# Kernel tuning notes

Measured on AMD Instinct MI355X. Metric: run time of the kernel, lower is better.

Reference implementation:

```python
import jax, jax.numpy as jnp
import numpy as np

NUM_SLOTS = 7
DIM = 4096
NUM_HEADS = 8
HEAD_DIM = DIM // NUM_HEADS
LN_EPS = 1e-5


def setup_inputs() -> dict:
    key = jax.random.key(0)
    ks = jax.random.split(key, 9)
    B, N = 8, 2048
    x = jax.random.normal(ks[0], (B, N, DIM), dtype=jnp.float32)
    slots = 1e-4 * jax.random.normal(ks[1], (NUM_SLOTS, DIM), dtype=jnp.float32)
    ln_g = jnp.ones((DIM,), jnp.float32)
    ln_b = jnp.zeros((DIM,), jnp.float32)
    # nn.MultiheadAttention packed in-projection: rows [Wq; Wk; Wv], each (DIM, DIM)
    s = 1.0 / np.sqrt(DIM)
    in_proj_w = jax.random.uniform(ks[2], (3 * DIM, DIM), jnp.float32, -s, s)
    in_proj_b = jnp.zeros((3 * DIM,), jnp.float32)
    out_proj_w = jax.random.uniform(ks[3], (DIM, DIM), jnp.float32, -s, s)
    out_proj_b = jnp.zeros((DIM,), jnp.float32)
    alpha = 0.1 * jax.random.normal(ks[4], (1,), jnp.float32)  # nonzero so gate path is active
    return {"x": x, "slots": slots, "ln_g": ln_g, "ln_b": ln_b,
            "in_proj_w": in_proj_w, "in_proj_b": in_proj_b,
            "out_proj_w": out_proj_w, "out_proj_b": out_proj_b, "alpha": alpha}


def _cmrm(x, slots, ln_g, ln_b, in_proj_w, in_proj_b, out_proj_w, out_proj_b, alpha):
    x32 = x.astype(jnp.float32)
    # pre LayerNorm
    mu = jnp.mean(x32, axis=-1, keepdims=True)
    var = jnp.mean(jnp.square(x32 - mu), axis=-1, keepdims=True)
    xn = (x32 - mu) * jax.lax.rsqrt(var + LN_EPS) * ln_g + ln_b  # (B,N,D)
    slots_c = jnp.clip(slots, -10.0, 10.0)  # (Q,D), Q=7
    Wq, Wk, Wv = jnp.split(in_proj_w, 3, axis=0)
    bq, bk, bv = jnp.split(in_proj_b, 3, axis=0)
    q = slots_c @ Wq.T + bq                      # (Q,D), identical for all batches
    k = xn @ Wk.T + bk                           # (B,N,D)
    v = xn @ Wv.T + bv                           # (B,N,D)
    B, N, _ = x.shape
    qh = q.reshape(NUM_SLOTS, NUM_HEADS, HEAD_DIM)          # (Q,H,hd)
    kh = k.reshape(B, N, NUM_HEADS, HEAD_DIM)
    vh = v.reshape(B, N, NUM_HEADS, HEAD_DIM)
    scale = 1.0 / np.sqrt(HEAD_DIM)
    scores = jnp.einsum('qhd,bnhd->bhqn', qh * scale, kh)   # (B,H,Q,N)
    attn = jax.nn.softmax(scores, axis=-1)
    ctx = jnp.einsum('bhqn,bnhd->bqhd', attn, vh).reshape(B, NUM_SLOTS, DIM)
    slots_out = ctx @ out_proj_w.T + out_proj_b             # (B,Q,D)
    slots_res = slots_c[None] + slots_out                   # residual, ungated slots
    gate = jnp.tanh(alpha)                                  # (1,)
    g = jnp.mean(gate * slots_res, axis=1, keepdims=True)   # (B,1,D)
    x_refined = (x32 + g).astype(x.dtype)
    attn_weights = jnp.mean(attn, axis=1)                   # torch avg over heads -> (B,Q,N)
    return x_refined, attn_weights


def reference(x, slots, ln_g, ln_b, in_proj_w, in_proj_b, out_proj_w, out_proj_b, alpha):
    return _cmrm(x, slots, ln_g, ln_b, in_proj_w, in_proj_b, out_proj_w, out_proj_b, alpha)
```

## Files before the change

### kernel.cpp

```cpp
#include <hip/hip_runtime.h>

typedef __attribute__((ext_vector_type(4))) float f32x4;
typedef __attribute__((ext_vector_type(8))) short short8x;

#define DIM   4096
#define NB    8
#define NN    2048
#define NROWS (NB*NN)
#define NHD   8
#define NQ    7
#define NHQ   56
#define SCALE 0.04419417382415922f

#define OFF_MU     0L
#define OFF_RSTD   16384L
#define OFF_Q7     32768L
#define OFF_SC7    61440L
#define OFF_U56    90112L
#define OFF_A      319488L
#define OFF_D0     319552L
#define OFF_SM     319616L
#define OFF_S1     323712L
#define OFF_CTXM   323776L
#define OFF_GFIN   356544L
#define OFF_YM     389312L
#define OFF_UGBF   651456L
#define OFF_STATP  782528L
#define OFF_SCT    913600L
#define OFF_BIG    1962176L
#define OFF_ATTN   (OFF_BIG)
#define OFF_AM     (OFF_BIG + 917504L)
#define OFF_PART   (OFF_BIG + 1048576L)

__device__ __forceinline__ unsigned short f2bf(float f) {
  union { float f; unsigned int u; } v; v.f = f;
  return (unsigned short)((v.u + 0x7FFFu + ((v.u >> 16) & 1u)) >> 16);
}
__device__ __forceinline__ unsigned short f2bfr(float f) {
  union { float f; unsigned int u; } v; v.f = f;
  return (unsigned short)((v.u + 0x8000u) >> 16);
}

__device__ __forceinline__ float blockSum256(float v, float* red) {
  #pragma unroll
  for (int m = 1; m < 64; m <<= 1) v += __shfl_xor(v, m);
  __syncthreads();
  if ((threadIdx.x & 63) == 0) red[threadIdx.x >> 6] = v;
  __syncthreads();
  return red[0] + red[1] + red[2] + red[3];
}
__device__ __forceinline__ float blockMax256(float v, float* red) {
  #pragma unroll
  for (int m = 1; m < 64; m <<= 1) v = fmaxf(v, __shfl_xor(v, m));
  __syncthreads();
  if ((threadIdx.x & 63) == 0) red[threadIdx.x >> 6] = v;
  __syncthreads();
  return fmaxf(fmaxf(red[0], red[1]), fmaxf(red[2], red[3]));
}

__global__ __launch_bounds__(256) void k_smean(const float* __restrict__ slots,
    float* __restrict__ sm, float* __restrict__ sc7) {
  int e = blockIdx.x * 256 + threadIdx.x;
  float s = 0;
  #pragma unroll
  for (int q = 0; q < 7; q++) {
    float v = fminf(fmaxf(slots[(long)q*DIM + e], -10.0f), 10.0f);
    sc7[(long)q*DIM + e] = v;
    s += v;
  }
  sm[e] = s * (1.0f / 7.0f);
}

__global__ __launch_bounds__(256) void k_qproj(const float* __restrict__ ipw,
    const float* __restrict__ ipb, const float* __restrict__ sc7, float* __restrict__ q7) {
  const int w = threadIdx.x >> 6, l = threadIdx.x & 63;
  const int d = blockIdx.x * 4 + w;
  const float4* wr4 = (const float4*)(ipw + (long)d * DIM);
  float acc[7] = {0,0,0,0,0,0,0};
  for (int e4 = l; e4 < 1024; e4 += 64) {
    float4 wv = wr4[e4];
    #pragma unroll
    for (int s = 0; s < 7; s++) {
      float4 sv = ((const float4*)(sc7 + (long)s*DIM))[e4];
      acc[s] += wv.x*sv.x + wv.y*sv.y + wv.z*sv.z + wv.w*sv.w;
    }
  }
  #pragma unroll
  for (int s = 0; s < 7; s++) {
    #pragma unroll
    for (int m = 1; m < 64; m <<= 1) acc[s] += __shfl_xor(acc[s], m);
  }
  if (l == 0) {
    float bq = ipb[d];
    #pragma unroll
    for (int s = 0; s < 7; s++) q7[(long)s*DIM + d] = acc[s] + bq;
  }
}

__global__ __launch_bounds__(256) void k_uproj(const float* __restrict__ ipw,
    const float* __restrict__ q7, float* __restrict__ upart) {
  const int h = blockIdx.y, c = blockIdx.z;
  const int e = blockIdx.x * 256 + threadIdx.x;
  __shared__ float qs[7][128];
  for (int i = threadIdx.x; i < 7*128; i += 256) {
    int s = i >> 7, hd = i & 127;
    qs[s][hd] = q7[(long)s*DIM + h*512 + c*128 + hd];
  }
  __syncthreads();
  float acc[7] = {0,0,0,0,0,0,0};
  const float* wp = ipw + ((long)(DIM + h*512 + c*128))*DIM + e;
  for (int hd = 0; hd < 128; hd++) {
    float wv = wp[(long)hd * DIM];
    #pragma unroll
    for (int s = 0; s < 7; s++) acc[s] += qs[s][hd] * wv;
  }
  #pragma unroll
  for (int s = 0; s < 7; s++) upart[(long)((c*8 + h)*7 + s)*DIM + e] = acc[s];
}

__global__ __launch_bounds__(256) void k_ured(const float* __restrict__ upart,
    const float* __restrict__ lng, float* __restrict__ u56, unsigned short* __restrict__ ugbf) {
  const int h = blockIdx.y;
  const int e = blockIdx.x * 256 + threadIdx.x;
  if (h == 8) {
    #pragma unroll
    for (int r = 0; r < 8; r++) ugbf[(long)(56 + r)*DIM + e] = 0;
    return;
  }
  float ge = lng[e];
  #pragma unroll
  for (int s = 0; s < 7; s++) {
    float u = 0;
    #pragma unroll
    for (int c = 0; c < 4; c++) u += upart[(long)((c*8 + h)*7 + s)*DIM + e];
    u *= SCALE;
    u56[(long)(h*7 + s)*DIM + e] = u;
    ugbf[(long)(h*7 + s)*DIM + e] = f2bf(u * ge);
  }
}

__global__ __launch_bounds__(256) void k_ad(const float* __restrict__ u56,
    const float* __restrict__ q7, const float* __restrict__ lng, const float* __restrict__ lnb,
    const float* __restrict__ ipb, float* __restrict__ Aarr, float* __restrict__ D0arr) {
  __shared__ float red[4];
  const int hq = blockIdx.x, h = hq / 7, q = hq % 7;
  float pa = 0, pd = 0, pc = 0;
  for (int e = threadIdx.x; e < DIM; e += 256) {
    float uv = u56[(long)hq*DIM + e];
    pa += uv * lng[e]; pd += uv * lnb[e];
  }
  for (int hd = threadIdx.x; hd < 512; hd += 256)
    pc += q7[(long)q*DIM + h*512 + hd] * ipb[DIM + h*512 + hd];
  pa = blockSum256(pa, red);
  pd = blockSum256(pd, red);
  pc = blockSum256(pc, red);
  if (threadIdx.x == 0) { Aarr[hq] = pa; D0arr[hq] = pd + SCALE * pc; }
}

__global__ __launch_bounds__(256) void k_scores2(const float* __restrict__ x,
    const unsigned short* __restrict__ ugbf, float* __restrict__ raw, float2* __restrict__ statp) {
  const int tid = threadIdx.x;
  const int w = tid >> 6, l = tid & 63;
  const int lr = l & 15, lk8 = (l >> 4) * 8;
  const int rowblk = blockIdx.x >> 2, ks = blockIdx.x & 3;
  const int row0w = rowblk * 64 + w * 16;
  const long arow = (long)(row0w + lr) * DIM;
  const int kbase = ks * 1024;
  f32x4 acc0 = {0,0,0,0}, acc1 = {0,0,0,0}, acc2 = {0,0,0,0}, acc3 = {0,0,0,0};
  float sx = 0.f, sxx = 0.f;
  const long b0 = (long)(0*16 + lr)*DIM, b1 = (long)(1*16 + lr)*DIM,
             b2 = (long)(2*16 + lr)*DIM, b3 = (long)(3*16 + lr)*DIM;
  #pragma unroll 2
  for (int kc = kbase; kc < kbase + 1024; kc += 32) {
    const float4 v0 = *(const float4*)(x + arow + kc + lk8);
    const float4 v1 = *(const float4*)(x + arow + kc + lk8 + 4);
    sx  += (v0.x + v0.y) + (v0.z + v0.w) + (v1.x + v1.y) + (v1.z + v1.w);
    sxx += v0.x*v0.x + v0.y*v0.y + v0.z*v0.z + v0.w*v0.w
         + v1.x*v1.x + v1.y*v1.y + v1.z*v1.z + v1.w*v1.w;
    short8x a;
    a[0] = (short)f2bfr(v0.x); a[1] = (short)f2bfr(v0.y);
    a[2] = (short)f2bfr(v0.z); a[3] = (short)f2bfr(v0.w);
    a[4] = (short)f2bfr(v1.x); a[5] = (short)f2bfr(v1.y);
    a[6] = (short)f2bfr(v1.z); a[7] = (short)f2bfr(v1.w);
    short8x bb0 = *(const short8x*)(ugbf + b0 + kc + lk8);
    acc0 = __builtin_amdgcn_mfma_f32_16x16x32_bf16(a, bb0, acc0, 0, 0, 0);
    short8x bb1 = *(const short8x*)(ugbf + b1 + kc + lk8);
    acc1 = __builtin_amdgcn_mfma_f32_16x16x32_bf16(a, bb1, acc1, 0, 0, 0);
    short8x bb2 = *(const short8x*)(ugbf + b2 + kc + lk8);
    acc2 = __builtin_amdgcn_mfma_f32_16x16x32_bf16(a, bb2, acc2, 0, 0, 0);
    short8x bb3 = *(const short8x*)(ugbf + b3 + kc + lk8);
    acc3 = __builtin_amdgcn_mfma_f32_16x16x32_bf16(a, bb3, acc3, 0, 0, 0);
  }
  sx += __shfl_xor(sx, 16);  sx += __shfl_xor(sx, 32);
  sxx += __shfl_xor(sxx, 16); sxx += __shfl_xor(sxx, 32);
  if (l < 16) {
    float2 p; p.x = sx; p.y = sxx;
    statp[(long)ks*NROWS + row0w + l] = p;
  }
  const long base = ((long)ks*NROWS + row0w) * 64;
  #pragma unroll
  for (int i = 0; i < 4; i++) {
    long ro = base + (long)((l >> 4)*4 + i) * 64 + lr;
    raw[ro +  0] = acc0[i];
    raw[ro + 16] = acc1[i];
    raw[ro + 32] = acc2[i];
    raw[ro + 48] = acc3[i];
  }
}

__global__ __launch_bounds__(256) void k_sepi(const float* __restrict__ raw,
    const float2* __restrict__ statp, const float* __restrict__ Aarr,
    const float* __restrict__ D0arr, float* __restrict__ mu_o, float* __restrict__ rstd_o,
    float* __restrict__ sct) {
  const int w = threadIdx.x >> 6, l = threadIdx.x & 63;
  const int row = blockIdx.x * 4 + w;
  float s = 0;
  #pragma unroll
  for (int ks = 0; ks < 4; ks++) s += raw[((long)ks*NROWS + row)*64 + l];
  float sx = 0, sxx = 0;
  #pragma unroll
  for (int ks = 0; ks < 4; ks++) {
    float2 p = statp[(long)ks*NROWS + row];
    sx += p.x; sxx += p.y;
  }
  float mu = sx * (1.0f/DIM), var = sxx * (1.0f/DIM) - mu*mu;
  float rs = rsqrtf(var + 1e-5f);
  if (l == 0) { mu_o[row] = mu; rstd_o[row] = rs; }
  if (l < NHQ) sct[(long)l*NROWS + row] = rs*(s - mu*Aarr[l]) + D0arr[l];
}

__global__ __launch_bounds__(256) void k_softmax(const float* __restrict__ sct,
    float* __restrict__ attn) {
  __shared__ float red[4];
  const int b = blockIdx.x / NHQ, hq = blockIdx.x % NHQ;
  const int tid = threadIdx.x;
  const float* sp = sct + (long)hq*NROWS + (long)b*NN;
  float s[8]; float mx = -3.4e38f;
  #pragma unroll
  for (int j = 0; j < 8; j++) { s[j] = sp[tid + j*256]; mx = fmaxf(mx, s[j]); }
  mx = blockMax256(mx, red);
  float sum = 0;
  #pragma unroll
  for (int j = 0; j < 8; j++) { s[j] = __expf(s[j] - mx); sum += s[j]; }
  sum = blockSum256(sum, red);
  float inv = 1.0f / sum;
  const int h = hq / NQ, q = hq % NQ;
  float* ap = attn + ((long)(b*NHD + h)*NQ + q)*NN;
  #pragma unroll
  for (int j = 0; j < 8; j++) ap[tid + j*256] = s[j] * inv;
}

__global__ __launch_bounds__(256) void k_means(const float* __restrict__ attn,
    float* __restrict__ am, float* __restrict__ out_attn) {
  const int b = blockIdx.x >> 3, nc = blockIdx.x & 7;
  const int n = nc*256 + threadIdx.x;
  float aq[7] = {0,0,0,0,0,0,0};
  #pragma unroll
  for (int h = 0; h < 8; h++) {
    float ah = 0;
    #pragma unroll
    for (int q = 0; q < 7; q++) {
      float v = attn[((long)(b*NHD + h)*NQ + q)*NN + n];
      aq[q] += v; ah += v;
    }
    am[((long)(b*NHD + h))*NN + n] = ah * (1.0f/7.0f);
  }
  #pragma unroll
  for (int q = 0; q < 7; q++) out_attn[((long)(b*NQ + q))*NN + n] = aq[q] * 0.125f;
}

__global__ __launch_bounds__(256) void k_s1(const float* __restrict__ am,
    const float* __restrict__ mu, const float* __restrict__ rstd, float* __restrict__ s1) {
  __shared__ float red[4];
  const int bh = blockIdx.x, b = bh >> 3;
  float p = 0;
  for (int n = threadIdx.x; n < NN; n += 256) {
    int row = b*NN + n;
    p += am[(long)bh*NN + n] * mu[row] * rstd[row];
  }
  p = blockSum256(p, red);
  if (threadIdx.x == 0) s1[bh] = p;
}

__global__ __launch_bounds__(256) void k_ypart(const float* __restrict__ x,
    const float* __restrict__ am, const float* __restrict__ rstd, float* __restrict__ part) {
  const int bid = blockIdx.x;
  const int b = bid >> 6, ec = (bid >> 4) & 3, nc = bid & 15;
  __shared__ float amr[8][128];
  const int tid = threadIdx.x;
  for (int i = tid; i < 1024; i += 256) {
    int h = i >> 7, nn = i & 127;
    int row = b*NN + nc*128 + nn;
    amr[h][nn] = am[((long)(b*NHD + h))*NN + nc*128 + nn] * rstd[row];
  }
  __syncthreads();
  const int e = ec*1024 + tid*4;
  float ax[8], ay[8], az[8], aw[8];
  #pragma unroll
  for (int h = 0; h < 8; h++) { ax[h]=0; ay[h]=0; az[h]=0; aw[h]=0; }
  const float* xp = x + ((long)(b*NN + nc*128))*DIM + e;
  #pragma unroll 2
  for (int nn = 0; nn < 128; nn++) {
    const float4 xv = *(const float4*)(xp + (long)nn*DIM);
    #pragma unroll
    for (int h = 0; h < 8; h++) {
      float a = amr[h][nn];
      ax[h] += a*xv.x; ay[h] += a*xv.y; az[h] += a*xv.z; aw[h] += a*xv.w;
    }
  }
  #pragma unroll
  for (int h = 0; h < 8; h++) {
    float4 o; o.x = ax[h]; o.y = ay[h]; o.z = az[h]; o.w = aw[h];
    *(float4*)&part[((long)(nc*64 + b*8 + h))*DIM + e] = o;
  }
}

__global__ __launch_bounds__(256) void k_yred(const float* __restrict__ part,
    const float* __restrict__ s1, const float* __restrict__ lng, const float* __restrict__ lnb,
    float* __restrict__ ym) {
  const long i4 = (long)blockIdx.x*256 + threadIdx.x;
  const float4* p4 = (const float4*)part;
  float4 s = p4[i4];
  #pragma unroll
  for (int nc = 1; nc < 16; nc++) {
    float4 v = p4[(long)nc*65536 + i4];
    s.x += v.x; s.y += v.y; s.z += v.z; s.w += v.w;
  }
  const int bh = (int)(i4 >> 10), e4 = (int)(i4 & 1023);
  float sv = s1[bh];
  float4 g = ((const float4*)lng)[e4], bb = ((const float4*)lnb)[e4];
  float4 o;
  o.x = g.x*(s.x - sv) + bb.x; o.y = g.y*(s.y - sv) + bb.y;
  o.z = g.z*(s.z - sv) + bb.z; o.w = g.w*(s.w - sv) + bb.w;
  ((float4*)ym)[i4] = o;
}

__global__ __launch_bounds__(256) void k_ctxm(const float* __restrict__ ipw,
    const float* __restrict__ ipb, const float* __restrict__ ym, float* __restrict__ ctxm) {
  const int w = threadIdx.x >> 6, l = threadIdx.x & 63;
  const int d = blockIdx.x*4 + w;
  const int h = d >> 9;
  const float4* wr4 = (const float4*)(ipw + ((long)(2*DIM + d))*DIM);
  float acc[8] = {0,0,0,0,0,0,0,0};
  for (int e4 = l; e4 < 1024; e4 += 64) {
    float4 wv = wr4[e4];
    #pragma unroll
    for (int b = 0; b < 8; b++) {
      float4 y = ((const float4*)(ym + (long)(b*8 + h)*DIM))[e4];
      acc[b] += wv.x*y.x + wv.y*y.y + wv.z*y.z + wv.w*y.w;
    }
  }
  #pragma unroll
  for (int b = 0; b < 8; b++) {
    #pragma unroll
    for (int m = 1; m < 64; m <<= 1) acc[b] += __shfl_xor(acc[b], m);
  }
  if (l == 0) {
    float bias = ipb[2*DIM + d];
    #pragma unroll
    for (int b = 0; b < 8; b++) ctxm[(long)b*DIM + d] = acc[b] + bias;
  }
}

__global__ __launch_bounds__(256) void k_gvec(const float* __restrict__ opw,
    const float* __restrict__ opb, const float* __restrict__ ctxm, const float* __restrict__ sm,
    const float* __restrict__ alpha, float* __restrict__ gfin) {
  const int w = threadIdx.x >> 6, l = threadIdx.x & 63;
  const int d = blockIdx.x*4 + w;
  const float4* wr4 = (const float4*)(opw + (long)d*DIM);
  float acc[8] = {0,0,0,0,0,0,0,0};
  for (int e4 = l; e4 < 1024; e4 += 64) {
    float4 wv = wr4[e4];
    #pragma unroll
    for (int b = 0; b < 8; b++) {
      float4 c = ((const float4*)(ctxm + (long)b*DIM))[e4];
      acc[b] += wv.x*c.x + wv.y*c.y + wv.z*c.z + wv.w*c.w;
    }
  }
  #pragma unroll
  for (int b = 0; b < 8; b++) {
    #pragma unroll
    for (int m = 1; m < 64; m <<= 1) acc[b] += __shfl_xor(acc[b], m);
  }
  if (l == 0) {
    float t = tanhf(alpha[0]);
    float base = sm[d] + opb[d];
    #pragma unroll
    for (int b = 0; b < 8; b++) gfin[(long)b*DIM + d] = t * (base + acc[b]);
  }
}

__global__ __launch_bounds__(256) void k_refine(const float* __restrict__ x,
    const float* __restrict__ gfin, float* __restrict__ out) {
  const float4* x4 = (const float4*)x;
  const float4* g4 = (const float4*)gfin;
  float4* o4 = (float4*)out;
  const long total = (long)NROWS * 1024;
  for (long i4 = (long)blockIdx.x*256 + threadIdx.x; i4 < total; i4 += (long)gridDim.x*256) {
    long b = i4 >> 21;
    long e4 = i4 & 1023;
    float4 xv = x4[i4], gv = g4[b*1024 + e4];
    float4 o; o.x = xv.x + gv.x; o.y = xv.y + gv.y; o.z = xv.z + gv.z; o.w = xv.w + gv.w;
    o4[i4] = o;
  }
}

extern "C" void kernel_launch(void* const* d_in, const int* in_sizes, int n_in,
                              void* d_out, int out_size, void* d_ws, size_t ws_size,
                              hipStream_t stream) {
  const float* x     = (const float*)d_in[0];
  const float* slots = (const float*)d_in[1];
  const float* lng   = (const float*)d_in[2];
  const float* lnb   = (const float*)d_in[3];
  const float* ipw   = (const float*)d_in[4];
  const float* ipb   = (const float*)d_in[5];
  const float* opw   = (const float*)d_in[6];
  const float* opb   = (const float*)d_in[7];
  const float* alpha = (const float*)d_in[8];
  float* out = (float*)d_out;
  float* ws  = (float*)d_ws;

  float* mu     = ws + OFF_MU;
  float* rstd   = ws + OFF_RSTD;
  float* q7     = ws + OFF_Q7;
  float* sc7    = ws + OFF_SC7;
  float* u56    = ws + OFF_U56;
  float* Aarr   = ws + OFF_A;
  float* D0arr  = ws + OFF_D0;
  float* sm     = ws + OFF_SM;
  float* s1     = ws + OFF_S1;
  float* ctxm   = ws + OFF_CTXM;
  float* gfin   = ws + OFF_GFIN;
  float* ym     = ws + OFF_YM;
  unsigned short* ugbf = (unsigned short*)(ws + OFF_UGBF);
  float2* statp = (float2*)(ws + OFF_STATP);
  float* sct    = ws + OFF_SCT;
  float* upart  = ws + OFF_BIG;
  float* raw    = ws + OFF_BIG;
  float* attn   = ws + OFF_ATTN;
  float* am     = ws + OFF_AM;
  float* part   = ws + OFF_PART;
  float* out_attn = out + (long)NROWS * DIM;

  hipLaunchKernelGGL(k_smean,   dim3(16),        dim3(256), 0, stream, slots, sm, sc7);
  hipLaunchKernelGGL(k_qproj,   dim3(1024),      dim3(256), 0, stream, ipw, ipb, sc7, q7);
  hipLaunchKernelGGL(k_uproj,   dim3(16, 8, 4),  dim3(256), 0, stream, ipw, q7, upart);
  hipLaunchKernelGGL(k_ured,    dim3(16, 9),     dim3(256), 0, stream, upart, lng, u56, ugbf);
  hipLaunchKernelGGL(k_ad,      dim3(56),        dim3(256), 0, stream, u56, q7, lng, lnb, ipb, Aarr, D0arr);
  hipLaunchKernelGGL(k_scores2, dim3(1024),      dim3(256), 0, stream, x, ugbf, raw, statp);
  hipLaunchKernelGGL(k_sepi,    dim3(4096),      dim3(256), 0, stream, raw, statp, Aarr, D0arr, mu, rstd, sct);
  hipLaunchKernelGGL(k_softmax, dim3(448),       dim3(256), 0, stream, sct, attn);
  hipLaunchKernelGGL(k_means,   dim3(64),        dim3(256), 0, stream, attn, am, out_attn);
  hipLaunchKernelGGL(k_s1,      dim3(64),        dim3(256), 0, stream, am, mu, rstd, s1);
  hipLaunchKernelGGL(k_ypart,   dim3(512),       dim3(256), 0, stream, x, am, rstd, part);
  hipLaunchKernelGGL(k_yred,    dim3(256),       dim3(256), 0, stream, part, s1, lng, lnb, ym);
  hipLaunchKernelGGL(k_ctxm,    dim3(1024),      dim3(256), 0, stream, ipw, ipb, ym, ctxm);
  hipLaunchKernelGGL(k_gvec,    dim3(1024),      dim3(256), 0, stream, opw, opb, ctxm, sm, alpha, gfin);
  hipLaunchKernelGGL(k_refine,  dim3(8192),      dim3(256), 0, stream, x, gfin, out);
}
```

Baseline: 406.4 us.

## Fuse small kernels and recompute softmax probabilities instead of materializing attn

Folds the slot clamp and mean into the q-projection and gvec kernels, merges the A/D0 reductions into k_ured via atomics, and replaces the full softmax write plus separate means and s1 kernels with a stats-only softmax followed by a fused kernel that recomputes probabilities and accumulates head means and s1. It also doubles the number of ypart blocks by halving the row chunk. The aim is to cut launch count and the round trip of the large attn intermediate. In exchange it adds float atomics, which make the summation order nondeterministic, and redoes the exp work in the second pass.

Result: slower. 425.3 us (+4.6%).

```diff
diff --git a/kernel.cpp b/kernel.cpp
--- a/kernel.cpp
+++ b/kernel.cpp
@@ -15,22 +15,19 @@
 #define OFF_MU     0L
 #define OFF_RSTD   16384L
 #define OFF_Q7     32768L
-#define OFF_SC7    61440L
-#define OFF_U56    90112L
-#define OFF_A      319488L
-#define OFF_D0     319552L
-#define OFF_SM     319616L
-#define OFF_S1     323712L
-#define OFF_CTXM   323776L
-#define OFF_GFIN   356544L
-#define OFF_YM     389312L
-#define OFF_UGBF   651456L
-#define OFF_STATP  782528L
-#define OFF_SCT    913600L
-#define OFF_BIG    1962176L
-#define OFF_ATTN   (OFF_BIG)
-#define OFF_AM     (OFF_BIG + 917504L)
-#define OFF_PART   (OFF_BIG + 1048576L)
+#define OFF_A      61440L
+#define OFF_D0     61504L
+#define OFF_S1     61568L
+#define OFF_SMST   61632L
+#define OFF_CTXM   62528L
+#define OFF_GFIN   95296L
+#define OFF_YM     128064L
+#define OFF_UGBF   390208L
+#define OFF_STATP  521280L
+#define OFF_SCT    652352L
+#define OFF_BIG    1700928L
+#define OFF_AM     (OFF_BIG)
+#define OFF_PART   (OFF_BIG + 131072L)
 
 __device__ __forceinline__ unsigned short f2bf(float f) {
   union { float f; unsigned int u; } v; v.f = f;
@@ -41,9 +38,13 @@
   return (unsigned short)((v.u + 0x8000u) >> 16);
 }
 
+__device__ __forceinline__ float waveSum(float v) {
+  #pragma unroll
+  for (int m = 1; m < 64; m <<= 1) v += __shfl_xor(v, m);
+  return v;
+}
 __device__ __forceinline__ float blockSum256(float v, float* red) {
-  #pragma unroll
-  for (int m = 1; m < 64; m <<= 1) v += __shfl_xor(v, m);
+  v = waveSum(v);
   __syncthreads();
   if ((threadIdx.x & 63) == 0) red[threadIdx.x >> 6] = v;
   __syncthreads();
@@ -58,21 +59,8 @@
   return fmaxf(fmaxf(red[0], red[1]), fmaxf(red[2], red[3]));
 }
 
-__global__ __launch_bounds__(256) void k_smean(const float* __restrict__ slots,
-    float* __restrict__ sm, float* __restrict__ sc7) {
-  int e = blockIdx.x * 256 + threadIdx.x;
-  float s = 0;
-  #pragma unroll
-  for (int q = 0; q < 7; q++) {
-    float v = fminf(fmaxf(slots[(long)q*DIM + e], -10.0f), 10.0f);
-    sc7[(long)q*DIM + e] = v;
-    s += v;
-  }
-  sm[e] = s * (1.0f / 7.0f);
-}
-
 __global__ __launch_bounds__(256) void k_qproj(const float* __restrict__ ipw,
-    const float* __restrict__ ipb, const float* __restrict__ sc7, float* __restrict__ q7) {
+    const float* __restrict__ ipb, const float* __restrict__ slots, float* __restrict__ q7) {
   const int w = threadIdx.x >> 6, l = threadIdx.x & 63;
   const int d = blockIdx.x * 4 + w;
   const float4* wr4 = (const float4*)(ipw + (long)d * DIM);
@@ -81,20 +69,29 @@
     float4 wv = wr4[e4];
     #pragma unroll
     for (int s = 0; s < 7; s++) {
-      float4 sv = ((const float4*)(sc7 + (long)s*DIM))[e4];
+      float4 sv = ((const float4*)(slots + (long)s*DIM))[e4];
+      sv.x = fminf(fmaxf(sv.x, -10.f), 10.f); sv.y = fminf(fmaxf(sv.y, -10.f), 10.f);
+      sv.z = fminf(fmaxf(sv.z, -10.f), 10.f); sv.w = fminf(fmaxf(sv.w, -10.f), 10.f);
       acc[s] += wv.x*sv.x + wv.y*sv.y + wv.z*sv.z + wv.w*sv.w;
     }
   }
   #pragma unroll
-  for (int s = 0; s < 7; s++) {
-    #pragma unroll
-    for (int m = 1; m < 64; m <<= 1) acc[s] += __shfl_xor(acc[s], m);
-  }
+  for (int s = 0; s < 7; s++) acc[s] = waveSum(acc[s]);
   if (l == 0) {
     float bq = ipb[d];
     #pragma unroll
     for (int s = 0; s < 7; s++) q7[(long)s*DIM + d] = acc[s] + bq;
   }
+}
+
+__global__ __launch_bounds__(64) void k_adinit(const float* __restrict__ q7,
+    const float* __restrict__ ipb, float* __restrict__ Aarr, float* __restrict__ D0arr) {
+  const int hq = blockIdx.x, h = hq / 7, q = hq % 7;
+  float acc = 0;
+  for (int i = threadIdx.x; i < 512; i += 64)
+    acc += q7[(long)q*DIM + h*512 + i] * ipb[DIM + h*512 + i];
+  acc = waveSum(acc);
+  if (threadIdx.x == 0) { Aarr[hq] = 0.f; D0arr[hq] = SCALE * acc; }
 }
 
 __global__ __launch_bounds__(256) void k_uproj(const float* __restrict__ ipw,
@@ -119,7 +116,8 @@
 }
 
 __global__ __launch_bounds__(256) void k_ured(const float* __restrict__ upart,
-    const float* __restrict__ lng, float* __restrict__ u56, unsigned short* __restrict__ ugbf) {
+    const float* __restrict__ lng, const float* __restrict__ lnb,
+    unsigned short* __restrict__ ugbf, float* __restrict__ Aarr, float* __restrict__ D0arr) {
   const int h = blockIdx.y;
   const int e = blockIdx.x * 256 + threadIdx.x;
   if (h == 8) {
@@ -127,34 +125,21 @@
     for (int r = 0; r < 8; r++) ugbf[(long)(56 + r)*DIM + e] = 0;
     return;
   }
-  float ge = lng[e];
+  float ge = lng[e], be = lnb[e];
   #pragma unroll
   for (int s = 0; s < 7; s++) {
     float u = 0;
     #pragma unroll
     for (int c = 0; c < 4; c++) u += upart[(long)((c*8 + h)*7 + s)*DIM + e];
     u *= SCALE;
-    u56[(long)(h*7 + s)*DIM + e] = u;
     ugbf[(long)(h*7 + s)*DIM + e] = f2bf(u * ge);
-  }
-}
-
-__global__ __launch_bounds__(256) void k_ad(const float* __restrict__ u56,
-    const float* __restrict__ q7, const float* __restrict__ lng, const float* __restrict__ lnb,
-    const float* __restrict__ ipb, float* __restrict__ Aarr, float* __restrict__ D0arr) {
-  __shared__ float red[4];
-  const int hq = blockIdx.x, h = hq / 7, q = hq % 7;
-  float pa = 0, pd = 0, pc = 0;
-  for (int e = threadIdx.x; e < DIM; e += 256) {
-    float uv = u56[(long)hq*DIM + e];
-    pa += uv * lng[e]; pd += uv * lnb[e];
-  }
-  for (int hd = threadIdx.x; hd < 512; hd += 256)
-    pc += q7[(long)q*DIM + h*512 + hd] * ipb[DIM + h*512 + hd];
-  pa = blockSum256(pa, red);
-  pd = blockSum256(pd, red);
-  pc = blockSum256(pc, red);
-  if (threadIdx.x == 0) { Aarr[hq] = pa; D0arr[hq] = pd + SCALE * pc; }
+    float pa = waveSum(u * ge);
+    float pd = waveSum(u * be);
+    if ((threadIdx.x & 63) == 0) {
+      atomicAdd(&Aarr[h*7 + s], pa);
+      atomicAdd(&D0arr[h*7 + s], pd);
+    }
+  }
 }
 
 __global__ __launch_bounds__(256) void k_scores2(const float* __restrict__ x,
@@ -229,9 +214,10 @@
   if (l < NHQ) sct[(long)l*NROWS + row] = rs*(s - mu*Aarr[l]) + D0arr[l];
 }
 
-__global__ __launch_bounds__(256) void k_softmax(const float* __restrict__ sct,
-    float* __restrict__ attn) {
+__global__ __launch_bounds__(256) void k_smax(const float* __restrict__ sct,
+    float2* __restrict__ stats, float* __restrict__ s1) {
   __shared__ float red[4];
+  if (blockIdx.x == 0 && threadIdx.x < 64) s1[threadIdx.x] = 0.f;
   const int b = blockIdx.x / NHQ, hq = blockIdx.x % NHQ;
   const int tid = threadIdx.x;
   const float* sp = sct + (long)hq*NROWS + (long)b*NN;
@@ -241,66 +227,59 @@
   mx = blockMax256(mx, red);
   float sum = 0;
   #pragma unroll
-  for (int j = 0; j < 8; j++) { s[j] = __expf(s[j] - mx); sum += s[j]; }
+  for (int j = 0; j < 8; j++) sum += __expf(s[j] - mx);
   sum = blockSum256(sum, red);
-  float inv = 1.0f / sum;
-  const int h = hq / NQ, q = hq % NQ;
-  float* ap = attn + ((long)(b*NHD + h)*NQ + q)*NN;
-  #pragma unroll
-  for (int j = 0; j < 8; j++) ap[tid + j*256] = s[j] * inv;
-}
-
-__global__ __launch_bounds__(256) void k_means(const float* __restrict__ attn,
-    float* __restrict__ am, float* __restrict__ out_attn) {
+  if (tid == 0) { float2 o; o.x = mx; o.y = 1.0f/sum; stats[b*NHQ + hq] = o; }
+}
+
+__global__ __launch_bounds__(256) void k_attnmeans(const float* __restrict__ sct,
+    const float2* __restrict__ stats, const float* __restrict__ mu, const float* __restrict__ rstd,
+    float* __restrict__ am, float* __restrict__ s1, float* __restrict__ out_attn) {
   const int b = blockIdx.x >> 3, nc = blockIdx.x & 7;
-  const int n = nc*256 + threadIdx.x;
+  const int tid = threadIdx.x;
+  const int n = nc*256 + tid, row = b*NN + n;
+  __shared__ float2 st[56];
+  if (tid < 56) st[tid] = stats[b*NHQ + tid];
+  __syncthreads();
+  const float mur = mu[row] * rstd[row];
   float aq[7] = {0,0,0,0,0,0,0};
   #pragma unroll
   for (int h = 0; h < 8; h++) {
     float ah = 0;
     #pragma unroll
     for (int q = 0; q < 7; q++) {
-      float v = attn[((long)(b*NHD + h)*NQ + q)*NN + n];
-      aq[q] += v; ah += v;
-    }
-    am[((long)(b*NHD + h))*NN + n] = ah * (1.0f/7.0f);
+      float2 s2 = st[h*7 + q];
+      float p = __expf(sct[(long)(h*7 + q)*NROWS + row] - s2.x) * s2.y;
+      aq[q] += p; ah += p;
+    }
+    float amv = ah * (1.0f/7.0f);
+    am[((long)(b*8 + h))*NN + n] = amv;
+    float sv = waveSum(amv * mur);
+    if ((tid & 63) == 0) atomicAdd(&s1[b*8 + h], sv);
   }
   #pragma unroll
   for (int q = 0; q < 7; q++) out_attn[((long)(b*NQ + q))*NN + n] = aq[q] * 0.125f;
-}
-
-__global__ __launch_bounds__(256) void k_s1(const float* __restrict__ am,
-    const float* __restrict__ mu, const float* __restrict__ rstd, float* __restrict__ s1) {
-  __shared__ float red[4];
-  const int bh = blockIdx.x, b = bh >> 3;
-  float p = 0;
-  for (int n = threadIdx.x; n < NN; n += 256) {
-    int row = b*NN + n;
-    p += am[(long)bh*NN + n] * mu[row] * rstd[row];
-  }
-  p = blockSum256(p, red);
-  if (threadIdx.x == 0) s1[bh] = p;
 }
 
 __global__ __launch_bounds__(256) void k_ypart(const float* __restrict__ x,
     const float* __restrict__ am, const float* __restrict__ rstd, float* __restrict__ part) {
   const int bid = blockIdx.x;
-  const int b = bid >> 6, ec = (bid >> 4) & 3, nc = bid & 15;
-  __shared__ float amr[8][128];
+  const int b = bid >> 7, ec = (bid >> 5) & 3, nc = bid & 31;
+  __shared__ float amr[8][64];
   const int tid = threadIdx.x;
-  for (int i = tid; i < 1024; i += 256) {
-    int h = i >> 7, nn = i & 127;
-    int row = b*NN + nc*128 + nn;
-    amr[h][nn] = am[((long)(b*NHD + h))*NN + nc*128 + nn] * rstd[row];
+  for (int i = tid; i < 512; i += 256) {
+    int h = i >> 6, nn = i & 63;
+    int row = b*NN + nc*64 + nn;
+    amr[h][nn] = am[((long)(b*8 + h))*NN + nc*64 + nn] * rstd[row];
   }
   __syncthreads();
   const int e = ec*1024 + tid*4;
   float ax[8], ay[8], az[8], aw[8];
   #pragma unroll
   for (int h = 0; h < 8; h++) { ax[h]=0; ay[h]=0; az[h]=0; aw[h]=0; }
-  const float* xp = x + ((long)(b*NN + nc*128))*DIM + e;
+  const float* xp = x + ((long)(b*NN + nc*64))*DIM + e;
   #pragma unroll 2
-  for (int nn = 0; nn < 128; nn++) {
+  for (int nn = 0; nn < 64; nn++) {
     const float4 xv = *(const float4*)(xp + (long)nn*DIM);
     #pragma unroll
     for (int h = 0; h < 8; h++) {
@@ -322,7 +301,7 @@
   const float4* p4 = (const float4*)part;
   float4 s = p4[i4];
   #pragma unroll
-  for (int nc = 1; nc < 16; nc++) {
+  for (int nc = 1; nc < 32; nc++) {
     float4 v = p4[(long)nc*65536 + i4];
     s.x += v.x; s.y += v.y; s.z += v.z; s.w += v.w;
   }
@@ -351,10 +330,7 @@
     }
   }
   #pragma unroll
-  for (int b = 0; b < 8; b++) {
-    #pragma unroll
-    for (int m = 1; m < 64; m <<= 1) acc[b] += __shfl_xor(acc[b], m);
-  }
+  for (int b = 0; b < 8; b++) acc[b] = waveSum(acc[b]);
   if (l == 0) {
     float bias = ipb[2*DIM + d];
     #pragma unroll
@@ -363,7 +339,7 @@
 }
 
 __global__ __launch_bounds__(256) void k_gvec(const float* __restrict__ opw,
-    const float* __restrict__ opb, const float* __restrict__ ctxm, const float* __restrict__ sm,
+    const float* __restrict__ opb, const float* __restrict__ ctxm, const float* __restrict__ slots,
     const float* __restrict__ alpha, float* __restrict__ gfin) {
   const int w = threadIdx.x >> 6, l = threadIdx.x & 63;
   const int d = blockIdx.x*4 + w;
@@ -378,13 +354,15 @@
     }
   }
   #pragma unroll
-  for (int b = 0; b < 8; b++) {
-    #pragma unroll
-    for (int m = 1; m < 64; m <<= 1) acc[b] += __shfl_xor(acc[b], m);
-  }
+  for (int b = 0; b < 8; b++) acc[b] = waveSum(acc[b]);
   if (l == 0) {
+    float smv = 0;
+    #pragma unroll
+    for (int q = 0; q < 7; q++)
+      smv += fminf(fmaxf(slots[(long)q*DIM + d], -10.f), 10.f);
+    smv *= (1.0f/7.0f);
     float t = tanhf(alpha[0]);
-    float base = sm[d] + opb[d];
+    float base = smv + opb[d];
     #pragma unroll
     for (int b = 0; b < 8; b++) gfin[(long)b*DIM + d] = t * (base + acc[b]);
   }
@@ -423,12 +401,10 @@
   float* mu     = ws + OFF_MU;
   float* rstd   = ws + OFF_RSTD;
   float* q7     = ws + OFF_Q7;
-  float* sc7    = ws + OFF_SC7;
-  float* u56    = ws + OFF_U56;
   float* Aarr   = ws + OFF_A;
   float* D0arr  = ws + OFF_D0;
-  float* sm     = ws + OFF_SM;
   float* s1     = ws + OFF_S1;
+  float2* stats = (float2*)(ws + OFF_SMST);
   float* ctxm   = ws + OFF_CTXM;
   float* gfin   = ws + OFF_GFIN;
   float* ym     = ws + OFF_YM;
@@ -437,24 +413,21 @@
   float* sct    = ws + OFF_SCT;
   float* upart  = ws + OFF_BIG;
   float* raw    = ws + OFF_BIG;
-  float* attn   = ws + OFF_ATTN;
   float* am     = ws + OFF_AM;
   float* part   = ws + OFF_PART;
   float* out_attn = out + (long)NROWS * DIM;
 
-  hipLaunchKernelGGL(k_smean,   dim3(16),        dim3(256), 0, stream, slots, sm, sc7);
-  hipLaunchKernelGGL(k_qproj,   dim3(1024),      dim3(256), 0, stream, ipw, ipb, sc7, q7);
-  hipLaunchKernelGGL(k_uproj,   dim3(16, 8, 4),  dim3(256), 0, stream, ipw, q7, upart);
-  hipLaunchKernelGGL(k_ured,    dim3(16, 9),     dim3(256), 0, stream, upart, lng, u56, ugbf);
-  hipLaunchKernelGGL(k_ad,      dim3(56),        dim3(256), 0, stream, u56, q7, lng, lnb, ipb, Aarr, D0arr);
-  hipLaunchKernelGGL(k_scores2, dim3(1024),      dim3(256), 0, stream, x, ugbf, raw, statp);
-  hipLaunchKernelGGL(k_sepi,    dim3(4096),      dim3(256), 0, stream, raw, statp, Aarr, D0arr, mu, rstd, sct);
-  hipLaunchKernelGGL(k_softmax, dim3(448),       dim3(256), 0, stream, sct, attn);
-  hipLaunchKernelGGL(k_means,   dim3(64),        dim3(256), 0, stream, attn, am, out_attn);
-  hipLaunchKernelGGL(k_s1,      dim3(64),        dim3(256), 0, stream, am, mu, rstd, s1);
-  hipLaunchKernelGGL(k_ypart,   dim3(512),       dim3(256), 0, stream, x, am, rstd, part);
-  hipLaunchKernelGGL(k_yred,    dim3(256),       dim3(256), 0, stream, part, s1, lng, lnb, ym);
-  hipLaunchKernelGGL(k_ctxm,    dim3(1024),      dim3(256), 0, stream, ipw, ipb, ym, ctxm);
-  hipLaunchKernelGGL(k_gvec,    dim3(1024),      dim3(256), 0, stream, opw, opb, ctxm, sm, alpha, gfin);
-  hipLaunchKernelGGL(k_refine,  dim3(8192),      dim3(256), 0, stream, x, gfin, out);
-}
+  hipLaunchKernelGGL(k_qproj,     dim3(1024),      dim3(256), 0, stream, ipw, ipb, slots, q7);
+  hipLaunchKernelGGL(k_adinit,    dim3(56),        dim3(64),  0, stream, q7, ipb, Aarr, D0arr);
+  hipLaunchKernelGGL(k_uproj,     dim3(16, 8, 4),  dim3(256), 0, stream, ipw, q7, upart);
+  hipLaunchKernelGGL(k_ured,      dim3(16, 9),     dim3(256), 0, stream, upart, lng, lnb, ugbf, Aarr, D0arr);
+  hipLaunchKernelGGL(k_scores2,   dim3(1024),      dim3(256), 0, stream, x, ugbf, raw, statp);
+  hipLaunchKernelGGL(k_sepi,      dim3(4096),      dim3(256), 0, stream, raw, statp, Aarr, D0arr, mu, rstd, sct);
+  hipLaunchKernelGGL(k_smax,      dim3(448),       dim3(256), 0, stream, sct, stats, s1);
+  hipLaunchKernelGGL(k_attnmeans, dim3(64),        dim3(256), 0, stream, sct, stats, mu, rstd, am, s1, out_attn);
+  hipLaunchKernelGGL(k_ypart,     dim3(1024),      dim3(256), 0, stream, x, am, rstd, part);
+  hipLaunchKernelGGL(k_yred,      dim3(256),       dim3(256), 0, stream, part, s1, lng, lnb, ym);
+  hipLaunchKernelGGL(k_ctxm,      dim3(1024),      dim3(256), 0, stream, ipw, ipb, ym, ctxm);
+  hipLaunchKernelGGL(k_gvec,      dim3(1024),      dim3(256), 0, stream, opw, opb, ctxm, slots, alpha, gfin);
+  hipLaunchKernelGGL(k_refine,    dim3(8192),      dim3(256), 0, stream, x, gfin, out);
+}
```
